# Performance work log

Hardware: AMD Instinct MI355X
Metric: run time of the kernel (lower is better)

The kernel has to match this reference:

```python
import jax, jax.numpy as jnp
import numpy as np

EPS = 1e-5

def _ln(x, w, b, axes):
    mu = jnp.mean(x, axis=axes, keepdims=True)
    var = jnp.mean((x - mu) ** 2, axis=axes, keepdims=True)
    return (x - mu) / jnp.sqrt(var + EPS) * w + b

def setup_inputs() -> dict:
    key = jax.random.key(0)
    ks = jax.random.split(key, 6)
    B, L, D, A, H, F = 1, 1024, 512, 32, 8, 2048
    s = 0.02
    return {
        "x": jax.random.normal(ks[0], (B, L, D), jnp.float32),
        "ln0_w": jnp.ones((D,), jnp.float32),
        "ln0_b": jnp.zeros((D,), jnp.float32),
        "ln1_w": jnp.ones((D, H), jnp.float32),
        "ln1_b": jnp.zeros((D, H), jnp.float32),
        "qw": jax.random.normal(ks[1], (D, A * H), jnp.float32) * s,
        "qb": jnp.zeros((A * H,), jnp.float32),
        "kw": jax.random.normal(ks[2], (D, A * H), jnp.float32) * s,
        "kb": jnp.zeros((A * H,), jnp.float32),
        "vw": jax.random.normal(ks[3], (D, D * H), jnp.float32) * s,
        "vb": jnp.zeros((D * H,), jnp.float32),
        "w1": jax.random.normal(ks[4], (D * H, F), jnp.float32) * s,
        "b1": jnp.zeros((F,), jnp.float32),
        "w2": jax.random.normal(ks[5], (F, D), jnp.float32) * s,
        "b2": jnp.zeros((D,), jnp.float32),
    }

def reference(x, ln0_w, ln0_b, ln1_w, ln1_b, qw, qb, kw, kb, vw, vb, w1, b1, w2, b2):
    B, L, D = x.shape
    H = ln1_w.shape[-1]
    _x = _ln(x, ln0_w, ln0_b, -1)
    # q, k: [B, L, d_att, H] with exp(clamp(.)) feature map
    q = jnp.exp(jnp.clip(_x @ qw + qb, -10.0, 10.0)).reshape(B, L, -1, H)
    k = jnp.exp(jnp.clip(_x @ kw + kb, -10.0, 10.0)).reshape(B, L, -1, H)
    # v uses raw x (not layernormed): [B, L, D, H]
    v = (x @ vw + vb).reshape(B, L, D, H)
    # cumulative outer-product KV state: [B, L, d_att, D, H]
    kv = jnp.cumsum(jnp.einsum('blah,bldh->bladh', k, v), axis=1)
    qkv = jnp.einsum('blah,bladh->bldh', q, kv)          # [B, L, D, H]
    den = jnp.einsum('blah,blah->blh', q, jnp.cumsum(k, axis=1))[..., None, :]  # [B, L, 1, H]
    y = x[..., None] + _ln(qkv / den, ln1_w, ln1_b, (-2, -1))  # LN over (D, H) jointly
    y = y.reshape(B, L, D * H)
    h1 = jax.nn.relu(y @ w1 + b1)
    return jax.nn.relu(h1 @ w2 + b2) + x
```

## Files before the change

kernel.cpp:

```cpp
#include <hip/hip_runtime.h>
#include <hip/hip_bf16.h>
#include <math.h>

#define L_SEQ 1024
#define D_DIM 512
#define A_DIM 32
#define H_DIM 8
#define F_DIM 2048
#define AH 256
#define DH 4096
#define NC 16
#define CH 64
#define EPS_LN 1e-5f

typedef __attribute__((ext_vector_type(8))) short short8;
typedef __attribute__((ext_vector_type(4))) short short4v;
typedef __attribute__((ext_vector_type(2))) short short2v;
typedef __attribute__((ext_vector_type(4))) float floatx4;

#define ASYNC_COPY16(gp, lp)                                                     \
    __builtin_amdgcn_global_load_lds(                                            \
        (const __attribute__((address_space(1))) void*)(const void*)(gp),        \
        (__attribute__((address_space(3))) void*)(void*)(lp), 16, 0, 0)

__global__ __launch_bounds__(256) void prep_kernel(const float* __restrict__ x,
                                                   const float* __restrict__ ln0w,
                                                   const float* __restrict__ ln0b,
                                                   const float* __restrict__ ln1w,
                                                   const float* __restrict__ ln1b,
                                                   const float* __restrict__ qw,
                                                   const float* __restrict__ kw,
                                                   const float* __restrict__ vw,
                                                   const float* __restrict__ w1,
                                                   const float* __restrict__ w2,
                                                   __hip_bfloat16* __restrict__ xn,
                                                   __hip_bfloat16* __restrict__ xb,
                                                   __hip_bfloat16* __restrict__ qkwt,
                                                   __hip_bfloat16* __restrict__ vwt,
                                                   __hip_bfloat16* __restrict__ w1t,
                                                   __hip_bfloat16* __restrict__ w2t,
                                                   float* __restrict__ wp,
                                                   float* __restrict__ bp) {
    __shared__ float tt[32][33];
    __shared__ float red[8];
    int bid = blockIdx.x;
    int tid = threadIdx.x;
    if (bid < 1024) {
        int l = bid;
        float v0 = x[l * D_DIM + tid];
        float v1 = x[l * D_DIM + 256 + tid];
        float s = v0 + v1, s2 = v0 * v0 + v1 * v1;
        for (int off = 32; off > 0; off >>= 1) {
            s += __shfl_down(s, off);
            s2 += __shfl_down(s2, off);
        }
        int lane = tid & 63, wid = tid >> 6;
        if (lane == 0) { red[wid] = s; red[4 + wid] = s2; }
        __syncthreads();
        float ts = red[0] + red[1] + red[2] + red[3];
        float t2 = red[4] + red[5] + red[6] + red[7];
        float mu = ts / (float)D_DIM;
        float var = t2 / (float)D_DIM - mu * mu;
        float rs = rsqrtf(var + EPS_LN);
        xn[l * D_DIM + tid]       = (__hip_bfloat16)((v0 - mu) * rs * ln0w[tid] + ln0b[tid]);
        xn[l * D_DIM + 256 + tid] = (__hip_bfloat16)((v1 - mu) * rs * ln0w[256 + tid] + ln0b[256 + tid]);
        xb[l * D_DIM + tid]       = (__hip_bfloat16)v0;
        xb[l * D_DIM + 256 + tid] = (__hip_bfloat16)v1;
        return;
    }
    if (bid == 12544) {
        int e0 = tid * 16;
        float o1[16], o2[16];
#pragma unroll
        for (int j = 0; j < 16; ++j) {
            int ee = e0 + j;
            int pi = ((ee & 511) << 3) | (ee >> 9);
            o1[j] = ln1w[pi];
            o2[j] = ln1b[pi];
        }
#pragma unroll
        for (int j = 0; j < 4; ++j) {
            *(float4*)(wp + e0 + j * 4) = *(float4*)&o1[j * 4];
            *(float4*)(bp + e0 + j * 4) = *(float4*)&o2[j * 4];
        }
        return;
    }
    const float* in;
    __hip_bfloat16* out;
    int R, C, mode = 0, t;
    if (bid < 1152)      { t = bid - 1024;  in = qw; out = qkwt;                      R = 512;  C = 256; }
    else if (bid < 1280) { t = bid - 1152;  in = kw; out = qkwt + (size_t)AH * D_DIM; R = 512;  C = 256; }
    else if (bid < 3328) { t = bid - 1280;  in = vw; out = vwt;  mode = 1;            R = 512;  C = 4096; }
    else if (bid < 11520){ t = bid - 3328;  in = w1; out = w1t;  mode = 2;            R = 4096; C = 2048; }
    else                 { t = bid - 11520; in = w2; out = w2t;                       R = 2048; C = 512; }
    int ctiles = C >> 5;
    int cx = t % ctiles, cy = t / ctiles;
    int r0 = cy * 32, c0 = cx * 32;
    {
        int r_in = tid >> 3, c4 = (tid & 7) * 4;
        int rr = r0 + r_in;
        if (mode == 2) rr = ((rr & 511) << 3) | (rr >> 9);
        float4 v = *(const float4*)(in + (size_t)rr * C + c0 + c4);
        tt[r_in][c4 + 0] = v.x;
        tt[r_in][c4 + 1] = v.y;
        tt[r_in][c4 + 2] = v.z;
        tt[r_in][c4 + 3] = v.w;
    }
    __syncthreads();
    {
        int c_out = tid >> 3, r4 = (tid & 7) * 4;
        int c = c0 + c_out;
        int orow = (mode == 1) ? (((c & 7) << 9) | (c >> 3)) : c;
        __hip_bfloat16 o[4];
#pragma unroll
        for (int j = 0; j < 4; ++j) o[j] = (__hip_bfloat16)tt[r4 + j][c_out];
        *(short4v*)(out + (size_t)orow * R + r0 + r4) = *(short4v*)o;
    }
}

template <int BN>
__device__ __forceinline__ void gemm_core(const __hip_bfloat16* __restrict__ A,
                                          const __hip_bfloat16* __restrict__ Bt,
                                          int K, int bm, int bn, int k_beg, int k_end,
                                          __hip_bfloat16* As, __hip_bfloat16* Bs,
                                          floatx4 (&acc)[2][BN / 32]) {
    constexpr int NT = BN / 32;
    const int tid = threadIdx.x;
    const int w = tid >> 6, lane = tid & 63;
    const int wm = (w >> 1) * 32, wn = (w & 1) * (BN / 2);
    const int quad = lane >> 4, l16 = lane & 15;
    const int srow = tid >> 4, sslot = tid & 15;
    const int scg = sslot ^ srow;
    for (int k0 = k_beg; k0 < k_end; k0 += 128) {
        __syncthreads();
#pragma unroll
        for (int j = 0; j < 4; ++j)
            ASYNC_COPY16(A + (size_t)(bm + j * 16 + srow) * K + k0 + scg * 8,
                         As + j * 2048 + w * 512);
#pragma unroll
        for (int j = 0; j < BN / 16; ++j)
            ASYNC_COPY16(Bt + (size_t)(bn + j * 16 + srow) * K + k0 + scg * 8,
                         Bs + j * 2048 + w * 512);
        __syncthreads();
#pragma unroll
        for (int ks = 0; ks < 4; ++ks) {
            short8 af[2], bfr[NT];
#pragma unroll
            for (int mt = 0; mt < 2; ++mt) {
                int rr = wm + mt * 16 + l16;
                af[mt] = *(const short8*)(As + rr * 128 + (((ks * 4 + quad) ^ (rr & 15)) * 8));
            }
#pragma unroll
            for (int nt = 0; nt < NT; ++nt) {
                int rr = wn + nt * 16 + l16;
                bfr[nt] = *(const short8*)(Bs + rr * 128 + (((ks * 4 + quad) ^ (rr & 15)) * 8));
            }
#pragma unroll
            for (int mt = 0; mt < 2; ++mt)
#pragma unroll
                for (int nt = 0; nt < NT; ++nt)
                    acc[mt][nt] = __builtin_amdgcn_mfma_f32_16x16x32_bf16(
                        af[mt], bfr[nt], acc[mt][nt], 0, 0, 0);
        }
    }
}

__global__ __launch_bounds__(256) void qkv_gemm(const __hip_bfloat16* __restrict__ xn,
                                                const __hip_bfloat16* __restrict__ xb,
                                                const __hip_bfloat16* __restrict__ qkwt,
                                                const __hip_bfloat16* __restrict__ vwt,
                                                const float* __restrict__ qb,
                                                const float* __restrict__ kb,
                                                const float* __restrict__ vb,
                                                __hip_bfloat16* __restrict__ q2,
                                                __hip_bfloat16* __restrict__ k2,
                                                __hip_bfloat16* __restrict__ vT) {
    __shared__ __align__(16) __hip_bfloat16 As[64 * 128];
    __shared__ __align__(16) __hip_bfloat16 Bs[64 * 128];
    const int tid = threadIdx.x;
    const int w = tid >> 6, lane = tid & 63;
    const int wm = (w >> 1) * 32, wn = (w & 1) * 32;
    const int quad = lane >> 4, l16 = lane & 15;
    int bid = blockIdx.x;
    bool isv = bid < 1024;
    const __hip_bfloat16 *A, *Bt;
    int bx, by;
    if (isv) {
        int r = bid >> 3;
        bx = (bid & 7) * 8 + (r & 7);
        by = r >> 3;
        A = xb; Bt = vwt;
    } else {
        int b2 = bid - 1024;
        bx = b2 & 7; by = b2 >> 3;
        A = xn; Bt = qkwt;
    }
    const int bm = by * 64, bn = bx * 64;
    floatx4 acc[2][2];
#pragma unroll
    for (int i = 0; i < 2; ++i)
#pragma unroll
        for (int j = 0; j < 2; ++j) acc[i][j] = (floatx4)0.f;
    gemm_core<64>(A, Bt, D_DIM, bm, bn, 0, D_DIM, As, Bs, acc);
    if (isv) {
        __syncthreads();
        __hip_bfloat16* Ct = As;
#pragma unroll
        for (int mt = 0; mt < 2; ++mt)
#pragma unroll
            for (int nt = 0; nt < 2; ++nt) {
                int col = bn + wn + nt * 16 + l16;
                int bi = ((col & 511) << 3) | (col >> 9);
                float bbv = vb[bi];
                __hip_bfloat16 tmp[4];
#pragma unroll
                for (int r = 0; r < 4; ++r)
                    tmp[r] = (__hip_bfloat16)(acc[mt][nt][r] + bbv);
                *(short4v*)&Ct[(wn + nt * 16 + l16) * 72 + wm + mt * 16 + quad * 4] =
                    *(short4v*)tmp;
            }
        __syncthreads();
        int colloc = tid >> 2, seg = (tid & 3) * 16;
        short8 o0 = *(const short8*)&Ct[colloc * 72 + seg];
        short8 o1 = *(const short8*)&Ct[colloc * 72 + seg + 8];
        *(short8*)(vT + (size_t)(bn + colloc) * 1024 + bm + seg) = o0;
        *(short8*)(vT + (size_t)(bn + colloc) * 1024 + bm + seg + 8) = o1;
    } else {
        __syncthreads();
        __hip_bfloat16* q2t = As;
        bool isq = bn < 256;
        const float* bias = isq ? qb : kb;
        int cb = isq ? bn : bn - 256;
#pragma unroll
        for (int mt = 0; mt < 2; ++mt)
#pragma unroll
            for (int nt = 0; nt < 2; ++nt) {
                int colloc = wn + nt * 16 + l16;
                float bb = bias[cb + colloc];
                int hh = colloc & 7, aa = colloc >> 3;
#pragma unroll
                for (int r = 0; r < 4; ++r) {
                    int rowloc = wm + mt * 16 + quad * 4 + r;
                    float val = expf(fminf(fmaxf(acc[mt][nt][r] + bb, -10.f), 10.f));
                    q2t[((hh * 64 + rowloc) << 3) + aa] = (__hip_bfloat16)val;
                }
            }
        __syncthreads();
        __hip_bfloat16* dst = isq ? q2 : k2;
        int a0 = cb >> 3;
#pragma unroll
        for (int j = 0; j < 2; ++j) {
            int p = tid + j * 256;
            int hh = p >> 6, ll = p & 63;
            short8 o = *(const short8*)&q2t[(hh * 64 + ll) << 3];
            *(short8*)(dst + (size_t)(hh * 1024 + bm + ll) * 32 + a0) = o;
        }
    }
}

__global__ __launch_bounds__(256) void w1_gemm(const __hip_bfloat16* __restrict__ y,
                                               const __hip_bfloat16* __restrict__ w1t,
                                               const float* __restrict__ b1,
                                               __hip_bfloat16* __restrict__ h1) {
    __shared__ __align__(16) __hip_bfloat16 As[64 * 128];
    __shared__ __align__(16) __hip_bfloat16 Bs[32 * 128];
    const int tid = threadIdx.x;
    const int w = tid >> 6, lane = tid & 63;
    const int wm = (w >> 1) * 32, wn = (w & 1) * 16;
    const int quad = lane >> 4, l16 = lane & 15;
    int bid = blockIdx.x;
    int r = bid >> 3;
    int bx = (bid & 7) * 8 + (r & 7);
    int by = r >> 3;
    const int bm = by * 64, bn = bx * 32;
    floatx4 acc[2][1];
    acc[0][0] = (floatx4)0.f;
    acc[1][0] = (floatx4)0.f;
    gemm_core<32>(y, w1t, DH, bm, bn, 0, DH, As, Bs, acc);
    int col = bn + wn + l16;
    float bb = b1[col];
#pragma unroll
    for (int mt = 0; mt < 2; ++mt)
#pragma unroll
        for (int rr = 0; rr < 4; ++rr) {
            int row = bm + wm + mt * 16 + quad * 4 + rr;
            h1[(size_t)row * F_DIM + col] =
                (__hip_bfloat16)fmaxf(acc[mt][0][rr] + bb, 0.f);
        }
}

__global__ __launch_bounds__(256) void w2_gemm(const __hip_bfloat16* __restrict__ h1,
                                               const __hip_bfloat16* __restrict__ w2t,
                                               const float* __restrict__ b2,
                                               const float* __restrict__ x,
                                               float* __restrict__ out) {
    __shared__ __align__(16) __hip_bfloat16 As[32 * 128];
    __shared__ __align__(16) __hip_bfloat16 Bs[64 * 128];
    const int tid = threadIdx.x;
    const int w = tid >> 6, lane = tid & 63;
    const int wm = (w >> 1) * 16, wn = (w & 1) * 32;
    const int quad = lane >> 4, l16 = lane & 15;
    const int srow = tid >> 4, sslot = tid & 15;
    const int scg = sslot ^ srow;
    int bid = blockIdx.x;
    const int bn = (bid & 7) * 64, bm = (bid >> 3) * 32;
    floatx4 acc[2];
    acc[0] = (floatx4)0.f;
    acc[1] = (floatx4)0.f;
    for (int k0 = 0; k0 < F_DIM; k0 += 128) {
        __syncthreads();
#pragma unroll
        for (int j = 0; j < 2; ++j)
            ASYNC_COPY16(h1 + (size_t)(bm + j * 16 + srow) * F_DIM + k0 + scg * 8,
                         As + j * 2048 + w * 512);
#pragma unroll
        for (int j = 0; j < 4; ++j)
            ASYNC_COPY16(w2t + (size_t)(bn + j * 16 + srow) * F_DIM + k0 + scg * 8,
                         Bs + j * 2048 + w * 512);
        __syncthreads();
#pragma unroll
        for (int ks = 0; ks < 4; ++ks) {
            int rra = wm + l16;
            short8 af = *(const short8*)(As + rra * 128 + (((ks * 4 + quad) ^ (rra & 15)) * 8));
#pragma unroll
            for (int nt = 0; nt < 2; ++nt) {
                int rr = wn + nt * 16 + l16;
                short8 bfr = *(const short8*)(Bs + rr * 128 + (((ks * 4 + quad) ^ (rr & 15)) * 8));
                acc[nt] = __builtin_amdgcn_mfma_f32_16x16x32_bf16(af, bfr, acc[nt], 0, 0, 0);
            }
        }
    }
#pragma unroll
    for (int nt = 0; nt < 2; ++nt)
#pragma unroll
        for (int r = 0; r < 4; ++r) {
            int row = bm + wm + quad * 4 + r;
            int col = bn + wn + nt * 16 + l16;
            out[(size_t)row * D_DIM + col] =
                fmaxf(acc[nt][r] + b2[col], 0.f) + x[(size_t)row * D_DIM + col];
        }
}

__global__ __launch_bounds__(256) void kvchunk_kernel(const __hip_bfloat16* __restrict__ k2,
                                                      const __hip_bfloat16* __restrict__ vT,
                                                      float* __restrict__ S,
                                                      float* __restrict__ Ka) {
    int c = blockIdx.x, h = blockIdx.y, dq = blockIdx.z;
    int tid = threadIdx.x;
    __shared__ __align__(16) __hip_bfloat16 kaT[32][72];
    __shared__ __align__(16) float St[128][36];
    {
        int l = tid >> 2, a0s = (tid & 3) * 8;
        short8 kv8 = *(const short8*)(k2 + (size_t)(h * 1024 + c * 64 + l) * 32 + a0s);
#pragma unroll
        for (int j = 0; j < 8; ++j)
            kaT[a0s + j][l] = ((const __hip_bfloat16*)&kv8)[j];
    }
    __syncthreads();
    int w = tid >> 6, lane = tid & 63, quad = lane >> 4, l16 = lane & 15;
    floatx4 acc[2][2];
#pragma unroll
    for (int i = 0; i < 2; ++i)
#pragma unroll
        for (int j = 0; j < 2; ++j) acc[i][j] = (floatx4)0.f;
#pragma unroll
    for (int ks = 0; ks < 2; ++ks) {
        short8 af[2], bfr[2];
#pragma unroll
        for (int mt = 0; mt < 2; ++mt)
            af[mt] = *(const short8*)&kaT[mt * 16 + l16][ks * 32 + quad * 8];
#pragma unroll
        for (int nt = 0; nt < 2; ++nt)
            bfr[nt] = *(const short8*)(vT + (size_t)(h * 512 + dq * 128 + w * 32 + nt * 16 + l16) * 1024
                                       + c * 64 + ks * 32 + quad * 8);
#pragma unroll
        for (int mt = 0; mt < 2; ++mt)
#pragma unroll
            for (int nt = 0; nt < 2; ++nt)
                acc[mt][nt] = __builtin_amdgcn_mfma_f32_16x16x32_bf16(
                    af[mt], bfr[nt], acc[mt][nt], 0, 0, 0);
    }
#pragma unroll
    for (int mt = 0; mt < 2; ++mt)
#pragma unroll
        for (int nt = 0; nt < 2; ++nt)
            *(floatx4*)&St[w * 32 + nt * 16 + l16][mt * 16 + quad * 4] = acc[mt][nt];
    __syncthreads();
    int d = tid >> 1, aseg = (tid & 1) * 16;
    float* dst = S + (size_t)((c * 8 + h) * 512 + dq * 128 + d) * 32 + aseg;
    const float* src = &St[d][aseg];
#pragma unroll
    for (int j = 0; j < 4; ++j)
        *(float4*)(dst + j * 4) = *(const float4*)(src + j * 4);
    if (dq == 0 && tid < 32) {
        float s = 0.f;
        for (int l = 0; l < CH; ++l) s += (float)kaT[tid][l];
        Ka[c * AH + tid * 8 + h] = s;
    }
}

__global__ __launch_bounds__(256) void scan_kernel(const float* __restrict__ S,
                                                   const float* __restrict__ Ka,
                                                   __hip_bfloat16* __restrict__ P2,
                                                   float* __restrict__ KaP) {
    size_t j = ((size_t)blockIdx.x * 256 + threadIdx.x) * 2;
    const size_t CS = 8 * 512 * 32;
    float2 run = {0.f, 0.f};
#pragma unroll
    for (int c = 0; c < NC; ++c) {
        __hip_bfloat16 o[2] = {(__hip_bfloat16)run.x, (__hip_bfloat16)run.y};
        *(short2v*)&P2[c * CS + j] = *(short2v*)o;
        float2 sv = *(const float2*)(S + c * CS + j);
        run.x += sv.x; run.y += sv.y;
    }
    if (blockIdx.x == 0) {
        int t = threadIdx.x;
        float rk = 0.f;
        for (int c = 0; c < NC; ++c) {
            KaP[c * AH + t] = rk;
            rk += Ka[c * AH + t];
        }
    }
}

__global__ __launch_bounds__(256) void passC_kernel(const __hip_bfloat16* __restrict__ q2,
                                                    const __hip_bfloat16* __restrict__ k2,
                                                    const __hip_bfloat16* __restrict__ vT,
                                                    const __hip_bfloat16* __restrict__ P2,
                                                    const float* __restrict__ KaP,
                                                    __hip_bfloat16* __restrict__ qkv,
                                                    float* __restrict__ den) {
    int c = blockIdx.x, h = blockIdx.y, dq = blockIdx.z;
    int tid = threadIdx.x;
    __shared__ __align__(16) __hip_bfloat16 Sc[64][72];
    __shared__ float KaPs[32];
    if (dq == 0 && tid < 32) KaPs[tid] = KaP[c * AH + tid * 8 + h];
    int w = tid >> 6, lane = tid & 63, quad = lane >> 4, l16 = lane & 15;
    const size_t qbase = (size_t)(h * 1024 + c * 64) * 32;
    short8 afq = *(const short8*)(q2 + qbase + (w * 16 + l16) * 32 + quad * 8);
    floatx4 sacc[4];
#pragma unroll
    for (int nt = 0; nt < 4; ++nt) sacc[nt] = (floatx4)0.f;
#pragma unroll
    for (int nt = 0; nt < 4; ++nt) {
        short8 bfr = *(const short8*)(k2 + qbase + (nt * 16 + l16) * 32 + quad * 8);
        sacc[nt] = __builtin_amdgcn_mfma_f32_16x16x32_bf16(afq, bfr, sacc[nt], 0, 0, 0);
    }
#pragma unroll
    for (int nt = 0; nt < 4; ++nt)
#pragma unroll
        for (int r = 0; r < 4; ++r) {
            int l = w * 16 + quad * 4 + r;
            int lp = nt * 16 + l16;
            Sc[l][lp] = (__hip_bfloat16)((lp <= l) ? sacc[nt][r] : 0.f);
        }
    __syncthreads();
    if (dq == 0 && tid < 64) {
        int l = tid;
        float s = 0.f;
        for (int lp = 0; lp <= l; ++lp) s += (float)Sc[l][lp];
        const __hip_bfloat16* qp = q2 + qbase + l * 32;
        for (int a = 0; a < A_DIM; ++a) s += (float)qp[a] * KaPs[a];
        den[(c * CH + l) * H_DIM + h] = s;
    }
    floatx4 acc[8];
#pragma unroll
    for (int nt = 0; nt < 8; ++nt) acc[nt] = (floatx4)0.f;
#pragma unroll
    for (int nt = 0; nt < 8; ++nt) {
        short8 pb = *(const short8*)(P2 + ((size_t)((c * 8 + h) * 512 + dq * 128 + nt * 16 + l16)) * 32 + quad * 8);
        acc[nt] = __builtin_amdgcn_mfma_f32_16x16x32_bf16(afq, pb, acc[nt], 0, 0, 0);
    }
#pragma unroll
    for (int ks = 0; ks < 2; ++ks) {
        short8 afs = *(const short8*)&Sc[w * 16 + l16][ks * 32 + quad * 8];
#pragma unroll
        for (int nt = 0; nt < 8; ++nt) {
            short8 bfr = *(const short8*)(vT + (size_t)(h * 512 + dq * 128 + nt * 16 + l16) * 1024
                                          + c * 64 + ks * 32 + quad * 8);
            acc[nt] = __builtin_amdgcn_mfma_f32_16x16x32_bf16(afs, bfr, acc[nt], 0, 0, 0);
        }
    }
#pragma unroll
    for (int nt = 0; nt < 8; ++nt)
#pragma unroll
        for (int r = 0; r < 4; ++r) {
            int l = w * 16 + quad * 4 + r;
            int d = dq * 128 + nt * 16 + l16;
            qkv[(size_t)(c * CH + l) * DH + h * D_DIM + d] = (__hip_bfloat16)acc[nt][r];
        }
}

__global__ __launch_bounds__(256) void ln1_kernel(const __hip_bfloat16* __restrict__ qkv,
                                                  const float* __restrict__ den,
                                                  const float* __restrict__ x,
                                                  const float* __restrict__ wp,
                                                  const float* __restrict__ bp,
                                                  __hip_bfloat16* __restrict__ y) {
    int l = blockIdx.x, tid = threadIdx.x;
    __shared__ float red[8];
    int h = tid >> 5;
    int e0 = tid * 16;
    int d0 = e0 & 511;
    float rden = 1.f / den[l * 8 + h];
    short8 v0 = *(const short8*)(qkv + (size_t)l * DH + e0);
    short8 v1 = *(const short8*)(qkv + (size_t)l * DH + e0 + 8);
    float vals[16];
    float s = 0.f, s2 = 0.f;
#pragma unroll
    for (int j = 0; j < 8; ++j) {
        vals[j] = (float)((const __hip_bfloat16*)&v0)[j] * rden;
        vals[8 + j] = (float)((const __hip_bfloat16*)&v1)[j] * rden;
    }
#pragma unroll
    for (int j = 0; j < 16; ++j) { s += vals[j]; s2 += vals[j] * vals[j]; }
    for (int off = 32; off > 0; off >>= 1) {
        s += __shfl_down(s, off);
        s2 += __shfl_down(s2, off);
    }
    int lane = tid & 63, wid = tid >> 6;
    if (lane == 0) { red[wid] = s; red[4 + wid] = s2; }
    __syncthreads();
    float ts = red[0] + red[1] + red[2] + red[3];
    float t2 = red[4] + red[5] + red[6] + red[7];
    float mu = ts / (float)DH;
    float var = t2 / (float)DH - mu * mu;
    float rs = rsqrtf(var + EPS_LN);
    __hip_bfloat16 o[16];
#pragma unroll
    for (int j4 = 0; j4 < 4; ++j4) {
        float4 xx = *(const float4*)(x + l * D_DIM + d0 + j4 * 4);
        float4 wv = *(const float4*)(wp + e0 + j4 * 4);
        float4 bv = *(const float4*)(bp + e0 + j4 * 4);
        o[j4 * 4 + 0] = (__hip_bfloat16)(xx.x + (vals[j4 * 4 + 0] - mu) * rs * wv.x + bv.x);
        o[j4 * 4 + 1] = (__hip_bfloat16)(xx.y + (vals[j4 * 4 + 1] - mu) * rs * wv.y + bv.y);
        o[j4 * 4 + 2] = (__hip_bfloat16)(xx.z + (vals[j4 * 4 + 2] - mu) * rs * wv.z + bv.z);
        o[j4 * 4 + 3] = (__hip_bfloat16)(xx.w + (vals[j4 * 4 + 3] - mu) * rs * wv.w + bv.w);
    }
    *(short8*)(y + (size_t)l * DH + e0) = *(short8*)&o[0];
    *(short8*)(y + (size_t)l * DH + e0 + 8) = *(short8*)&o[8];
}

extern "C" void kernel_launch(void* const* d_in, const int* in_sizes, int n_in,
                              void* d_out, int out_size, void* d_ws, size_t ws_size,
                              hipStream_t stream) {
    const float* x     = (const float*)d_in[0];
    const float* ln0_w = (const float*)d_in[1];
    const float* ln0_b = (const float*)d_in[2];
    const float* ln1_w = (const float*)d_in[3];
    const float* ln1_b = (const float*)d_in[4];
    const float* qw    = (const float*)d_in[5];
    const float* qb    = (const float*)d_in[6];
    const float* kw    = (const float*)d_in[7];
    const float* kb    = (const float*)d_in[8];
    const float* vw    = (const float*)d_in[9];
    const float* vb    = (const float*)d_in[10];
    const float* w1    = (const float*)d_in[11];
    const float* b1    = (const float*)d_in[12];
    const float* w2    = (const float*)d_in[13];
    const float* b2    = (const float*)d_in[14];
    float* out = (float*)d_out;

    char* ws = (char*)d_ws;
    __hip_bfloat16* xn_bf = (__hip_bfloat16*)(ws + 0);
    __hip_bfloat16* xbf   = (__hip_bfloat16*)(ws + 1048576);
    __hip_bfloat16* qkwt  = (__hip_bfloat16*)(ws + 2097152);
    __hip_bfloat16* vwt   = (__hip_bfloat16*)(ws + 2621440);
    __hip_bfloat16* w1t   = (__hip_bfloat16*)(ws + 6815744);
    __hip_bfloat16* w2t   = (__hip_bfloat16*)(ws + 23592960);
    __hip_bfloat16* q2    = (__hip_bfloat16*)(ws + 25690112);
    __hip_bfloat16* k2    = (__hip_bfloat16*)(ws + 26214400);
    __hip_bfloat16* vT    = (__hip_bfloat16*)(ws + 26738688);
    float* S              = (float*)(ws + 35127296);
    __hip_bfloat16* P2    = (__hip_bfloat16*)(ws + 43515904);
    __hip_bfloat16* qkvb  = (__hip_bfloat16*)(ws + 51904512);
    float* Ka  = (float*)(ws + 60293120);
    float* KaP = (float*)(ws + 60309504);
    float* den = (float*)(ws + 60325888);
    float* wp  = (float*)(ws + 60358656);
    float* bp  = (float*)(ws + 60375040);
    __hip_bfloat16* y  = P2;
    __hip_bfloat16* h1 = (__hip_bfloat16*)S;

    prep_kernel<<<12545, 256, 0, stream>>>(x, ln0_w, ln0_b, ln1_w, ln1_b,
                                           qw, kw, vw, w1, w2,
                                           xn_bf, xbf, qkwt, vwt, w1t, w2t, wp, bp);
    qkv_gemm<<<1152, 256, 0, stream>>>(xn_bf, xbf, qkwt, vwt, qb, kb, vb, q2, k2, vT);
    kvchunk_kernel<<<dim3(NC, H_DIM, 4), 256, 0, stream>>>(k2, vT, S, Ka);
    scan_kernel<<<256, 256, 0, stream>>>(S, Ka, P2, KaP);
    passC_kernel<<<dim3(NC, H_DIM, 4), 256, 0, stream>>>(q2, k2, vT, P2, KaP, qkvb, den);
    ln1_kernel<<<L_SEQ, 256, 0, stream>>>(qkvb, den, x, wp, bp, y);
    w1_gemm<<<1024, 256, 0, stream>>>(y, w1t, b1, h1);
    w2_gemm<<<256, 256, 0, stream>>>(h1, w2t, b2, x, out);

    (void)in_sizes; (void)n_in; (void)out_size; (void)ws_size;
}
```

Before: 206.1 us.

## Fuse chunk-state prefix scan into passC and drop separate scan kernel

Removes the scan kernel that computed exclusive prefix sums of per-chunk KV states and key sums. Each passC block now sums the preceding chunks' fp32 states from S itself and converts to bf16 before the MFMA. This saves a launch and the P2/KaP write-read round trip, but later chunks re-read up to 15 prior chunk states, so total global reads grow quadratically with chunk index and work becomes unbalanced across blocks.

```diff
diff --git a/kernel.cpp b/kernel.cpp
--- a/kernel.cpp
+++ b/kernel.cpp
@@ -15,7 +15,6 @@
 
 typedef __attribute__((ext_vector_type(8))) short short8;
 typedef __attribute__((ext_vector_type(4))) short short4v;
-typedef __attribute__((ext_vector_type(2))) short short2v;
 typedef __attribute__((ext_vector_type(4))) float floatx4;
 
 #define ASYNC_COPY16(gp, lp)                                                     \
@@ -399,42 +398,22 @@
     }
 }
 
-__global__ __launch_bounds__(256) void scan_kernel(const float* __restrict__ S,
-                                                   const float* __restrict__ Ka,
-                                                   __hip_bfloat16* __restrict__ P2,
-                                                   float* __restrict__ KaP) {
-    size_t j = ((size_t)blockIdx.x * 256 + threadIdx.x) * 2;
-    const size_t CS = 8 * 512 * 32;
-    float2 run = {0.f, 0.f};
-#pragma unroll
-    for (int c = 0; c < NC; ++c) {
-        __hip_bfloat16 o[2] = {(__hip_bfloat16)run.x, (__hip_bfloat16)run.y};
-        *(short2v*)&P2[c * CS + j] = *(short2v*)o;
-        float2 sv = *(const float2*)(S + c * CS + j);
-        run.x += sv.x; run.y += sv.y;
-    }
-    if (blockIdx.x == 0) {
-        int t = threadIdx.x;
-        float rk = 0.f;
-        for (int c = 0; c < NC; ++c) {
-            KaP[c * AH + t] = rk;
-            rk += Ka[c * AH + t];
-        }
-    }
-}
-
 __global__ __launch_bounds__(256) void passC_kernel(const __hip_bfloat16* __restrict__ q2,
                                                     const __hip_bfloat16* __restrict__ k2,
                                                     const __hip_bfloat16* __restrict__ vT,
-                                                    const __hip_bfloat16* __restrict__ P2,
-                                                    const float* __restrict__ KaP,
+                                                    const float* __restrict__ S,
+                                                    const float* __restrict__ Ka,
                                                     __hip_bfloat16* __restrict__ qkv,
                                                     float* __restrict__ den) {
     int c = blockIdx.x, h = blockIdx.y, dq = blockIdx.z;
     int tid = threadIdx.x;
     __shared__ __align__(16) __hip_bfloat16 Sc[64][72];
     __shared__ float KaPs[32];
-    if (dq == 0 && tid < 32) KaPs[tid] = KaP[c * AH + tid * 8 + h];
+    if (dq == 0 && tid < 32) {
+        float kc = 0.f;
+        for (int cc = 0; cc < c; ++cc) kc += Ka[cc * AH + tid * 8 + h];
+        KaPs[tid] = kc;
+    }
     int w = tid >> 6, lane = tid & 63, quad = lane >> 4, l16 = lane & 15;
     const size_t qbase = (size_t)(h * 1024 + c * 64) * 32;
     short8 afq = *(const short8*)(q2 + qbase + (w * 16 + l16) * 32 + quad * 8);
@@ -466,10 +445,21 @@
     floatx4 acc[8];
 #pragma unroll
     for (int nt = 0; nt < 8; ++nt) acc[nt] = (floatx4)0.f;
+    const size_t CS = (size_t)8 * 512 * 32;
 #pragma unroll
     for (int nt = 0; nt < 8; ++nt) {
-        short8 pb = *(const short8*)(P2 + ((size_t)((c * 8 + h) * 512 + dq * 128 + nt * 16 + l16)) * 32 + quad * 8);
-        acc[nt] = __builtin_amdgcn_mfma_f32_16x16x32_bf16(afq, pb, acc[nt], 0, 0, 0);
+        size_t base = ((size_t)(h * 512 + dq * 128 + nt * 16 + l16)) * 32 + quad * 8;
+        float p[8] = {0.f, 0.f, 0.f, 0.f, 0.f, 0.f, 0.f, 0.f};
+        for (int cc = 0; cc < c; ++cc) {
+            float4 a0 = *(const float4*)(S + cc * CS + base);
+            float4 a1 = *(const float4*)(S + cc * CS + base + 4);
+            p[0] += a0.x; p[1] += a0.y; p[2] += a0.z; p[3] += a0.w;
+            p[4] += a1.x; p[5] += a1.y; p[6] += a1.z; p[7] += a1.w;
+        }
+        __hip_bfloat16 pb8[8];
+#pragma unroll
+        for (int j = 0; j < 8; ++j) pb8[j] = (__hip_bfloat16)p[j];
+        acc[nt] = __builtin_amdgcn_mfma_f32_16x16x32_bf16(afq, *(short8*)pb8, acc[nt], 0, 0, 0);
     }
 #pragma unroll
     for (int ks = 0; ks < 2; ++ks) {
@@ -572,14 +562,12 @@
     __hip_bfloat16* k2    = (__hip_bfloat16*)(ws + 26214400);
     __hip_bfloat16* vT    = (__hip_bfloat16*)(ws + 26738688);
     float* S              = (float*)(ws + 35127296);
-    __hip_bfloat16* P2    = (__hip_bfloat16*)(ws + 43515904);
     __hip_bfloat16* qkvb  = (__hip_bfloat16*)(ws + 51904512);
     float* Ka  = (float*)(ws + 60293120);
-    float* KaP = (float*)(ws + 60309504);
     float* den = (float*)(ws + 60325888);
     float* wp  = (float*)(ws + 60358656);
     float* bp  = (float*)(ws + 60375040);
-    __hip_bfloat16* y  = P2;
+    __hip_bfloat16* y  = (__hip_bfloat16*)(ws + 43515904);
     __hip_bfloat16* h1 = (__hip_bfloat16*)S;
 
     prep_kernel<<<12545, 256, 0, stream>>>(x, ln0_w, ln0_b, ln1_w, ln1_b,
@@ -587,8 +575,7 @@
                                            xn_bf, xbf, qkwt, vwt, w1t, w2t, wp, bp);
     qkv_gemm<<<1152, 256, 0, stream>>>(xn_bf, xbf, qkwt, vwt, qb, kb, vb, q2, k2, vT);
     kvchunk_kernel<<<dim3(NC, H_DIM, 4), 256, 0, stream>>>(k2, vT, S, Ka);
-    scan_kernel<<<256, 256, 0, stream>>>(S, Ka, P2, KaP);
-    passC_kernel<<<dim3(NC, H_DIM, 4), 256, 0, stream>>>(q2, k2, vT, P2, KaP, qkvb, den);
+    passC_kernel<<<dim3(NC, H_DIM, 4), 256, 0, stream>>>(q2, k2, vT, S, Ka, qkvb, den);
     ln1_kernel<<<L_SEQ, 256, 0, stream>>>(qkvb, den, x, wp, bp, y);
     w1_gemm<<<1024, 256, 0, stream>>>(y, w1t, b1, h1);
     w2_gemm<<<256, 256, 0, stream>>>(h1, w2t, b2, x, out);
```

New measurement: 254.6 us. 23.5% more time.
